# Kernel tuning notes

Hardware: AMD Instinct MI355X
Metric: run time of the kernel (lower is better)

## Reference

```python
import jax, jax.numpy as jnp
import numpy as np

C_S, C_Z, C_OUT = 384, 128, 1


def setup_inputs() -> dict:
    key = jax.random.key(0)
    k_s, k_z, k_w = jax.random.split(key, 3)
    b, n = 1, 512
    s = jax.random.normal(k_s, (b, n, C_S), dtype=jnp.float32)
    z = jax.random.normal(k_z, (b, n, n, C_Z), dtype=jnp.float32)
    # Linear(2*c_s + c_z -> c_out); 'final' init is zeros in OpenFold, use
    # small random weights so gradients are non-trivial.
    W = jax.random.normal(k_w, (2 * C_S + C_Z, C_OUT), dtype=jnp.float32) * 0.02
    bias = jnp.zeros((C_OUT,), dtype=jnp.float32)
    return {"s": s, "z": z, "W": W, "b": bias, "start_ligand_ind": 384}


def reference(s, z, W, b, start_ligand_ind):
    # Decompose the linear over the concat [s_i, s_j, z] into three
    # projections; mathematically identical to cat+Linear but avoids
    # materializing the (b, n, n, 2*c_s + c_z) intermediate.
    W_i = W[:C_S]            # (c_s, c_out)
    W_j = W[C_S:2 * C_S]     # (c_s, c_out)
    W_z = W[2 * C_S:]        # (c_z, c_out)
    a_i = jnp.einsum('bnc,co->bno', s, W_i)          # (b, n, c_out)
    a_j = jnp.einsum('bnc,co->bno', s, W_j)          # (b, n, c_out)
    a_z = jnp.einsum('bnmc,co->bnmo', z, W_z)        # (b, n, n, c_out)
    logits = a_i[:, :, None, :] + a_j[:, None, :, :] + a_z + b
    logits = logits + jnp.swapaxes(logits, 1, 2)     # symmetrize over (i, j)
    return logits[:, :start_ligand_ind, start_ligand_ind:]
```

## Files before the change

### kernel.cpp

```cpp
#include <hip/hip_runtime.h>


#define C_S   384
#define C_Z   128
#define N_TOK 512
#define SL    384
#define M_OUT (N_TOK - SL)

__global__ void icn_as_kernel(const float* __restrict__ s,
                              const float* __restrict__ W,
                              float* __restrict__ a_s) {
    const int wave = (int)((blockIdx.x * blockDim.x + threadIdx.x) >> 6);
    const int lane = (int)(threadIdx.x & 63);
    if (wave >= N_TOK) return;
    const float* srow = s + (size_t)wave * C_S;
    float sum = 0.f;
    #pragma unroll
    for (int c0 = 0; c0 < C_S; c0 += 64) {
        const int c = c0 + lane;
        sum += srow[c] * (W[c] + W[C_S + c]);
    }
    #pragma unroll
    for (int off = 32; off; off >>= 1) sum += __shfl_down(sum, off, 64);
    if (lane == 0) a_s[wave] = sum;
}

__global__ void icn_main_kernel(const float* __restrict__ z,
                                const float* __restrict__ W,
                                const float* __restrict__ bias,
                                const float* __restrict__ a_s,
                                float* __restrict__ out) {
    const int g    = (int)((blockIdx.x * blockDim.x + threadIdx.x) >> 6);
    const int lane = (int)(threadIdx.x & 63);
    const int n = g >> 7;
    const int j = g & 127;
    const int m = SL + j;

    const float2* z_nm = (const float2*)(z + ((size_t)n * N_TOK + m) * C_Z);
    const float2* z_mn = (const float2*)(z + ((size_t)m * N_TOK + n) * C_Z);
    const float2* wz   = (const float2*)(W + 2 * C_S);

    const float2 v1 = z_nm[lane];
    const float2 v2 = z_mn[lane];
    const float2 w  = wz[lane];

    float sum = (v1.x + v2.x) * w.x + (v1.y + v2.y) * w.y;
    #pragma unroll
    for (int off = 32; off; off >>= 1) sum += __shfl_down(sum, off, 64);

    if (lane == 0) {
        out[g] = sum + a_s[n] + a_s[m] + 2.0f * bias[0];
    }
}

extern "C" void kernel_launch(void* const* d_in, const int* in_sizes, int n_in,
                              void* d_out, int out_size, void* d_ws, size_t ws_size,
                              hipStream_t stream) {
    const float* s    = (const float*)d_in[0];
    const float* z    = (const float*)d_in[1];
    const float* W    = (const float*)d_in[2];
    const float* bias = (const float*)d_in[3];

    float* a_s = (float*)d_ws;

    icn_as_kernel<<<dim3((N_TOK * 64) / 256), 256, 0, stream>>>(s, W, a_s);

    icn_main_kernel<<<dim3((SL * M_OUT) / 4), 256, 0, stream>>>(z, W, bias, a_s, (float*)d_out);
}
```

Baseline: 20.43 us.

## Fuse s-projection into main kernel and process two outputs per wave

Drops the separate a_s precompute kernel and instead recomputes the s·(W_i+W_j) dot products inside each wave of the main kernel, removing one launch and the dependency between the two kernels. Each wave now produces two adjacent outputs, using float4 loads where each half-wave reads one of the z_nm/z_mn rows, and writes a float2 result. The cost is redundant recomputation of the s projections for n, m0 and m1 in every wave, which adds loads of s rows from cache and extra FMAs per output.

New measurement: 19.55 us. 4.3% less time.

```diff
diff --git a/kernel.cpp b/kernel.cpp
--- a/kernel.cpp
+++ b/kernel.cpp
@@ -5,51 +5,67 @@
 #define C_Z   128
 #define N_TOK 512
 #define SL    384
-#define M_OUT (N_TOK - SL)
 
-__global__ void icn_as_kernel(const float* __restrict__ s,
-                              const float* __restrict__ W,
-                              float* __restrict__ a_s) {
-    const int wave = (int)((blockIdx.x * blockDim.x + threadIdx.x) >> 6);
+__global__ __launch_bounds__(256)
+void icn_fused_kernel(const float* __restrict__ s,
+                      const float* __restrict__ z,
+                      const float* __restrict__ W,
+                      const float* __restrict__ bias,
+                      float* __restrict__ out) {
+    const int tid  = (int)(blockIdx.x * blockDim.x + threadIdx.x);
+    const int wid  = tid >> 6;
     const int lane = (int)(threadIdx.x & 63);
-    if (wave >= N_TOK) return;
-    const float* srow = s + (size_t)wave * C_S;
-    float sum = 0.f;
+    const int g0   = wid << 1;
+    const int n    = g0 >> 7;
+    const int j0   = g0 & 127;
+    const int m0   = SL + j0;
+    const int m1   = m0 + 1;
+
+    const int  l  = lane & 31;
+    const bool lo = lane < 32;
+    const float4* zp0 = (const float4*)(z + (lo ? ((size_t)n  * N_TOK + m0)
+                                                : ((size_t)m0 * N_TOK + n)) * C_Z);
+    const float4* zp1 = (const float4*)(z + (lo ? ((size_t)n  * N_TOK + m1)
+                                                : ((size_t)m1 * N_TOK + n)) * C_Z);
+    const float4 v0 = zp0[l];
+    const float4 v1 = zp1[l];
+    const float4 wz = ((const float4*)(W + 2 * C_S))[l];
+
+    float p0 = v0.x * wz.x + v0.y * wz.y + v0.z * wz.z + v0.w * wz.w;
+    float p1 = v1.x * wz.x + v1.y * wz.y + v1.z * wz.z + v1.w * wz.w;
+
+    const float2* s2  = (const float2*)s;
+    const float2* W2  = (const float2*)W;
+    const float2* sn  = s2 + (size_t)n  * (C_S / 2);
+    const float2* sm0 = s2 + (size_t)m0 * (C_S / 2);
+    const float2* sm1 = s2 + (size_t)m1 * (C_S / 2);
+    float tn = 0.f, tm0 = 0.f, tm1 = 0.f;
     #pragma unroll
-    for (int c0 = 0; c0 < C_S; c0 += 64) {
-        const int c = c0 + lane;
-        sum += srow[c] * (W[c] + W[C_S + c]);
+    for (int k = 0; k < 3; ++k) {
+        const int c = lane + 64 * k;
+        const float2 wa = W2[c];
+        const float2 wb = W2[c + C_S / 2];
+        const float  wx = wa.x + wb.x, wy = wa.y + wb.y;
+        const float2 an = sn[c], a0 = sm0[c], a1 = sm1[c];
+        tn  += an.x * wx + an.y * wy;
+        tm0 += a0.x * wx + a0.y * wy;
+        tm1 += a1.x * wx + a1.y * wy;
     }
+    p0 += tn + tm0;
+    p1 += tn + tm1;
+
     #pragma unroll
-    for (int off = 32; off; off >>= 1) sum += __shfl_down(sum, off, 64);
-    if (lane == 0) a_s[wave] = sum;
-}
-
-__global__ void icn_main_kernel(const float* __restrict__ z,
-                                const float* __restrict__ W,
-                                const float* __restrict__ bias,
-                                const float* __restrict__ a_s,
-                                float* __restrict__ out) {
-    const int g    = (int)((blockIdx.x * blockDim.x + threadIdx.x) >> 6);
-    const int lane = (int)(threadIdx.x & 63);
-    const int n = g >> 7;
-    const int j = g & 127;
-    const int m = SL + j;
-
-    const float2* z_nm = (const float2*)(z + ((size_t)n * N_TOK + m) * C_Z);
-    const float2* z_mn = (const float2*)(z + ((size_t)m * N_TOK + n) * C_Z);
-    const float2* wz   = (const float2*)(W + 2 * C_S);
-
-    const float2 v1 = z_nm[lane];
-    const float2 v2 = z_mn[lane];
-    const float2 w  = wz[lane];
-
-    float sum = (v1.x + v2.x) * w.x + (v1.y + v2.y) * w.y;
-    #pragma unroll
-    for (int off = 32; off; off >>= 1) sum += __shfl_down(sum, off, 64);
+    for (int off = 32; off; off >>= 1) {
+        p0 += __shfl_down(p0, off, 64);
+        p1 += __shfl_down(p1, off, 64);
+    }
 
     if (lane == 0) {
-        out[g] = sum + a_s[n] + a_s[m] + 2.0f * bias[0];
+        const float bb = 2.0f * bias[0];
+        float2 r;
+        r.x = p0 + bb;
+        r.y = p1 + bb;
+        *(float2*)(out + g0) = r;
     }
 }
 
@@ -61,9 +77,5 @@
     const float* W    = (const float*)d_in[2];
     const float* bias = (const float*)d_in[3];
 
-    float* a_s = (float*)d_ws;
-
-    icn_as_kernel<<<dim3((N_TOK * 64) / 256), 256, 0, stream>>>(s, W, a_s);
-
-    icn_main_kernel<<<dim3((SL * M_OUT) / 4), 256, 0, stream>>>(z, W, bias, a_s, (float*)d_out);
+    icn_fused_kernel<<<dim3(6144), 256, 0, stream>>>(s, z, W, bias, (float*)d_out);
 }
```

## Process four output pairs per wavefront with float4 loads and vector store

Applied to the files above, without the earlier changes.

Each wavefront now computes four consecutive output elements instead of one, loading the contiguous z[n, m0..m0+3] rows as float4 and the four transposed rows split across half-waves. The reduction becomes 32-lane xor shuffles for two values per half, and results are written as a single float4 store. The bias is folded into a_s in the first kernel. This cuts the wave count fourfold and widens memory transactions, but each wave does more serial work and the grid shrinks to 3072 blocks.

New measurement: 18.43 us. 1.11x faster.

```diff
diff --git a/kernel.cpp b/kernel.cpp
--- a/kernel.cpp
+++ b/kernel.cpp
@@ -5,11 +5,12 @@
 #define C_Z   128
 #define N_TOK 512
 #define SL    384
-#define M_OUT (N_TOK - SL)
 
-__global__ void icn_as_kernel(const float* __restrict__ s,
-                              const float* __restrict__ W,
-                              float* __restrict__ a_s) {
+__global__ __launch_bounds__(256)
+void icn_as_kernel(const float* __restrict__ s,
+                   const float* __restrict__ W,
+                   const float* __restrict__ bias,
+                   float* __restrict__ a_s) {
     const int wave = (int)((blockIdx.x * blockDim.x + threadIdx.x) >> 6);
     const int lane = (int)(threadIdx.x & 63);
     if (wave >= N_TOK) return;
@@ -22,34 +23,59 @@
     }
     #pragma unroll
     for (int off = 32; off; off >>= 1) sum += __shfl_down(sum, off, 64);
-    if (lane == 0) a_s[wave] = sum;
+    if (lane == 0) a_s[wave] = sum + bias[0];
 }
 
-__global__ void icn_main_kernel(const float* __restrict__ z,
-                                const float* __restrict__ W,
-                                const float* __restrict__ bias,
-                                const float* __restrict__ a_s,
-                                float* __restrict__ out) {
-    const int g    = (int)((blockIdx.x * blockDim.x + threadIdx.x) >> 6);
+__global__ __launch_bounds__(256)
+void icn_main_kernel(const float* __restrict__ z,
+                     const float* __restrict__ W,
+                     const float* __restrict__ a_s,
+                     float* __restrict__ out) {
+    const int tid  = (int)(blockIdx.x * blockDim.x + threadIdx.x);
+    const int wid  = tid >> 6;
     const int lane = (int)(threadIdx.x & 63);
-    const int n = g >> 7;
-    const int j = g & 127;
-    const int m = SL + j;
+    const int g0   = wid << 2;
+    const int n    = g0 >> 7;
+    const int j0   = g0 & 127;
+    const int m0   = SL + j0;
 
-    const float2* z_nm = (const float2*)(z + ((size_t)n * N_TOK + m) * C_Z);
-    const float2* z_mn = (const float2*)(z + ((size_t)m * N_TOK + n) * C_Z);
-    const float2* wz   = (const float2*)(W + 2 * C_S);
+    const int  l  = lane & 31;
+    const bool lo = lane < 32;
 
-    const float2 v1 = z_nm[lane];
-    const float2 v2 = z_mn[lane];
-    const float2 w  = wz[lane];
+    const float4 wz = ((const float4*)(W + 2 * C_S))[l];
 
-    float sum = (v1.x + v2.x) * w.x + (v1.y + v2.y) * w.y;
+    const float4* za = (const float4*)(z + ((size_t)n * N_TOK + m0) * C_Z);
+    const float4 a0 = za[lane];
+    const float4 a1 = za[lane + 64];
+
+    const size_t zb_n = (size_t)n * C_Z;
+    const float4* b0p = (const float4*)(z + ((size_t)(lo ? m0 : m0 + 1) * N_TOK) * C_Z + zb_n);
+    const float4* b1p = (const float4*)(z + ((size_t)(lo ? m0 + 2 : m0 + 3) * N_TOK) * C_Z + zb_n);
+    const float4 b0 = b0p[l];
+    const float4 b1 = b1p[l];
+
+    float r0 = (a0.x + b0.x) * wz.x + (a0.y + b0.y) * wz.y
+             + (a0.z + b0.z) * wz.z + (a0.w + b0.w) * wz.w;
+    float r1 = (a1.x + b1.x) * wz.x + (a1.y + b1.y) * wz.y
+             + (a1.z + b1.z) * wz.z + (a1.w + b1.w) * wz.w;
+
     #pragma unroll
-    for (int off = 32; off; off >>= 1) sum += __shfl_down(sum, off, 64);
+    for (int off = 16; off; off >>= 1) {
+        r0 += __shfl_xor(r0, off, 64);
+        r1 += __shfl_xor(r1, off, 64);
+    }
 
+    const float j1 = __shfl(r0, 32, 64);
+    const float j3 = __shfl(r1, 32, 64);
     if (lane == 0) {
-        out[g] = sum + a_s[n] + a_s[m] + 2.0f * bias[0];
+        const float an = a_s[n];
+        const float4 am = *(const float4*)(a_s + m0);
+        float4 o;
+        o.x = r0 + an + am.x;
+        o.y = j1 + an + am.y;
+        o.z = r1 + an + am.z;
+        o.w = j3 + an + am.w;
+        *(float4*)(out + g0) = o;
     }
 }
 
@@ -63,7 +89,7 @@
 
     float* a_s = (float*)d_ws;
 
-    icn_as_kernel<<<dim3((N_TOK * 64) / 256), 256, 0, stream>>>(s, W, a_s);
+    icn_as_kernel<<<dim3((N_TOK * 64) / 256), 256, 0, stream>>>(s, W, bias, a_s);
 
-    icn_main_kernel<<<dim3((SL * M_OUT) / 4), 256, 0, stream>>>(z, W, bias, a_s, (float*)d_out);
+    icn_main_kernel<<<dim3(3072), 256, 0, stream>>>(z, W, a_s, (float*)d_out);
 }
```
